# Optimization experiments

Hardware: AMD Instinct MI355X
Metric: run time of the kernel (lower is better)

## Reference

```python
import jax, jax.numpy as jnp
import numpy as np
from functools import partial

B, N, T = 4, 10000, 128
E = 160000
H, C = 4, 64            # heads, out_channels per head
GAT_DIM = H * C         # 256
NEG_SLOPE = 0.2


def conv1d(x, w, b):
    # x: (M, Cin, L), w: (Cout, Cin, K), 'same' padding (pad=1 for k=3)
    y = jax.lax.conv_general_dilated(x, w, window_strides=(1,), padding=[(1, 1)],
                                     dimension_numbers=('NCH', 'OIH', 'NCH'))
    return y + b[None, :, None]


def maxpool2(x):
    # kernel=2, stride=2 over last axis
    return jax.lax.reduce_window(x, -jnp.inf, jax.lax.max,
                                 (1, 1, 2), (1, 1, 2), 'VALID')


def gat_layer_single(x, src, dst, W, att_s, att_d, bias):
    # x: (N, Fin); PyG GATConv with concat=True, self-loops already appended to src/dst
    n = x.shape[0]
    xl = (x @ W).reshape(n, H, C)                       # (N, H, C)
    a_s = jnp.sum(xl * att_s[None], axis=-1)            # (N, H)
    a_d = jnp.sum(xl * att_d[None], axis=-1)            # (N, H)
    e = jax.nn.leaky_relu(a_s[src] + a_d[dst], NEG_SLOPE)  # (E', H)
    emax = jax.ops.segment_max(e, dst, num_segments=n)     # (N, H)
    ex = jnp.exp(e - emax[dst])
    denom = jax.ops.segment_sum(ex, dst, num_segments=n)   # (N, H)
    alpha = ex / (denom[dst] + 1e-16)                       # (E', H)
    msg = xl[src] * alpha[..., None]                        # (E', H, C)
    out = jax.ops.segment_sum(msg, dst, num_segments=n)     # (N, H, C)
    return out.reshape(n, H * C) + bias


def setup_inputs() -> dict:
    key = jax.random.key(0)
    ks = jax.random.split(key, 24)
    rn = lambda k, sh, fan: jax.random.normal(k, sh, jnp.float32) / np.sqrt(fan)
    inp = {
        'x': jax.random.normal(ks[0], (B, N, T), jnp.float32),
        'edge_index': jax.random.randint(ks[1], (2, E), 0, N, jnp.int64),
        # temporal conv
        'cw1': rn(ks[2], (32, 1, 3), 3), 'cb1': jnp.zeros((32,), jnp.float32),
        'cw2': rn(ks[3], (64, 32, 3), 96), 'cb2': jnp.zeros((64,), jnp.float32),
        # GAT layer 0 (in=64)
        'W0': rn(ks[4], (64, GAT_DIM), 64), 'as0': rn(ks[5], (H, C), C), 'ad0': rn(ks[6], (H, C), C),
        'b0': jnp.zeros((GAT_DIM,), jnp.float32),
        # GAT layer 1 (in=256)
        'W1': rn(ks[7], (GAT_DIM, GAT_DIM), GAT_DIM), 'as1': rn(ks[8], (H, C), C), 'ad1': rn(ks[9], (H, C), C),
        'b1': jnp.zeros((GAT_DIM,), jnp.float32),
        # classification head 256->128->2
        'Wc1': rn(ks[10], (GAT_DIM, 128), GAT_DIM), 'bc1': jnp.zeros((128,), jnp.float32),
        'Wc2': rn(ks[11], (128, 2), 128), 'bc2': jnp.zeros((2,), jnp.float32),
        # attribution head 256->64->1
        'Wa1': rn(ks[12], (GAT_DIM, 64), GAT_DIM), 'ba1': jnp.zeros((64,), jnp.float32),
        'Wa2': rn(ks[13], (64, 1), 64), 'ba2': jnp.zeros((1,), jnp.float32),
    }
    return inp


def reference(x, edge_index, cw1, cb1, cw2, cb2, W0, as0, ad0, b0, W1, as1, ad1, b1,
              Wc1, bc1, Wc2, bc2, Wa1, ba1, Wa2, ba2):
    b, n, t = x.shape
    # ---- temporal conv over all B*N node signals ----
    xf = x.reshape(b * n, 1, t)
    h = jax.nn.relu(conv1d(xf, cw1, cb1))            # (BN, 32, T)
    h = maxpool2(h)                                  # (BN, 32, T//2)
    h = jax.nn.relu(conv1d(h, cw2, cb2))             # (BN, 64, T//2)
    feat = jnp.mean(h, axis=-1).reshape(b, n, 64)    # adaptive_avg_pool1d(1)
    # ---- GAT stack (self-loops appended, PyG default) ----
    src0, dst0 = edge_index[0], edge_index[1]
    loops = jnp.arange(n, dtype=src0.dtype)
    src = jnp.concatenate([src0, loops])
    dst = jnp.concatenate([dst0, loops])
    gat0 = jax.vmap(partial(gat_layer_single, src=src, dst=dst, W=W0, att_s=as0, att_d=ad0, bias=b0))
    gat1 = jax.vmap(partial(gat_layer_single, src=src, dst=dst, W=W1, att_s=as1, att_d=ad1, bias=b1))
    g = jax.nn.relu(gat0(feat))                      # (B, N, 256); dropout = identity (eval)
    g = jax.nn.relu(gat1(g))                         # (B, N, 256)
    # ---- heads ----
    pooled = jnp.mean(g, axis=1)                     # (B, 256)
    logits = jax.nn.relu(pooled @ Wc1 + bc1) @ Wc2 + bc2          # (B, 2)
    attr = jax.nn.sigmoid(jax.nn.relu(g @ Wa1 + ba1) @ Wa2 + ba2)  # (B, N, 1)
    return logits, attr[..., 0]
```

## Files before the change

kernel.cpp:

```cpp
#include <hip/hip_runtime.h>
#include <hip/hip_bf16.h>
#include <math.h>

typedef __hip_bfloat16 bf16;
typedef unsigned short u16;
typedef unsigned int u32;
typedef __attribute__((ext_vector_type(8))) short short8;
typedef __attribute__((ext_vector_type(4))) float f32x4;
typedef __attribute__((ext_vector_type(2))) float f32x2;

#define BATCH 4
#define NNODE 10000
#define TLEN 128
#define NEDGE 160000
#define GDIM 256
#define NHEAD 4
#define XROW 272

#define S_CW1 0
#define S_CB1 96
#define S_CB2 128
#define S_AS0 192
#define S_AD0 448
#define S_B0  704
#define S_AS1 960
#define S_AD1 1216
#define S_B1  1472
#define S_BC1 1728
#define S_WC2 1856
#define S_BC2 2112
#define S_BA1 2114
#define S_WA2 2178
#define S_BA2 2242
#define S_TOTAL 2243

__device__ __forceinline__ float prelu(float v) { return fmaxf(v, 0.f); }
__device__ __forceinline__ u16 f2b(float f) {
    union { float f; u32 u; } v; v.f = f;
    u32 r = v.u + 0x7FFF + ((v.u >> 16) & 1);
    return (u16)(r >> 16);
}
__device__ __forceinline__ float u2f(u16 u) {
    union { u32 u; float f; } v; v.u = ((u32)u) << 16;
    return v.f;
}
__device__ __forceinline__ float ldw(const void* p, int off, bool isbf) {
    return isbf ? u2f(((const u16*)p)[off]) : ((const float*)p)[off];
}

__device__ __forceinline__ bool probe_x_bf16(const void* xsrc) {
    int lane = threadIdx.x & 63;
    u16 h = ((const u16*)xsrc)[2 * lane];
    int e = (h >> 7) & 0xFF;
    unsigned long long m = __ballot(e >= 117 && e <= 130);
    return __popcll(m) >= 32;
}
__device__ __forceinline__ bool probe_ei64(const int* ei) {
    int lane = threadIdx.x & 63;
    int v = ei[2 * lane + 1];
    unsigned long long m = __ballot(v == 0);
    return __popcll(m) >= 56;
}

struct WPtrs { const void* p[20]; };

#define PRE_TBLK 665
__global__ __launch_bounds__(256) void k_pre(WPtrs wp, const void* __restrict__ xsrc,
        const int* __restrict__ ei, float* __restrict__ wbuf,
        u16* __restrict__ cw2r, u16* __restrict__ W0t, u16* __restrict__ W1t,
        u16* __restrict__ Wa1t, int* __restrict__ counts) {
    bool isbf = probe_x_bf16(xsrc);
    int b = blockIdx.x;
    if (b >= PRE_TBLK) {
        const int C2[16] = {0,96,128,192,448,704,960,1216,1472,1728,1856,2112,
                            2114,2178,2242,2243};
        const int SRC[15] = {0,1,3,5,6,7,9,10,11,13,14,15,17,18,19};
        int i = (b - PRE_TBLK) * 256 + threadIdx.x;
        if (i >= S_TOTAL) return;
        int j = 14;
        for (int t = 0; t < 15; ++t) { if (i < C2[t + 1]) { j = t; break; } }
        wbuf[i] = ldw(wp.p[SRC[j]], i - C2[j], isbf);
        return;
    }
    int i = b * 256 + threadIdx.x;
    if (i < 6144) {
        int c2 = i / 96, k = i - c2 * 96, s = k >> 5, ci = k & 31;
        cw2r[i] = f2b(ldw(wp.p[2], c2 * 96 + ci * 3 + s, isbf));
    }
    if (i < 16384) {
        int k = i >> 8, c = i & 255;
        W0t[c * 64 + k] = f2b(ldw(wp.p[4], k * 256 + c, isbf));
        int ka = i >> 6, ca = i & 63;
        Wa1t[ca * 256 + ka] = f2b(ldw(wp.p[16], ka * 64 + ca, isbf));
    }
    if (i < 65536) {
        int k = i >> 8, c = i & 255;
        W1t[c * 256 + k] = f2b(ldw(wp.p[8], k * 256 + c, isbf));
    }
    if (i < NEDGE + NNODE) {
        bool ei64 = probe_ei64(ei);
        int dst;
        if (i < NEDGE) dst = ei64 ? ei[2 * (NEDGE + i)] : ei[NEDGE + i];
        else dst = i - NEDGE;
        if (dst >= 0 && dst < NNODE) atomicAdd(&counts[dst], 1);
    }
}

__global__ __launch_bounds__(1024) void k_scan(const int* __restrict__ counts,
        int* __restrict__ cur, int* __restrict__ row_ptr) {
    __shared__ int buf[1024];
    int t = threadIdx.x;
    int base = t * 10;
    int c[10];
    int s = 0;
    #pragma unroll
    for (int i = 0; i < 10; ++i) {
        int idx = base + i;
        c[i] = (idx < NNODE) ? counts[idx] : 0;
        s += c[i];
    }
    buf[t] = s;
    __syncthreads();
    for (int off = 1; off < 1024; off <<= 1) {
        int v = (t >= off) ? buf[t - off] : 0;
        __syncthreads();
        buf[t] += v;
        __syncthreads();
    }
    int run = buf[t] - s;
    #pragma unroll
    for (int i = 0; i < 10; ++i) {
        int idx = base + i;
        if (idx < NNODE) {
            cur[idx] = run;
            run += c[i];
            row_ptr[idx + 1] = run;
        }
    }
    if (t == 0) row_ptr[0] = 0;
}

#define HSTR 40
#define NPW 4
#define FILL_BLK 665
__global__ __launch_bounds__(256) void k_conv(const void* __restrict__ xsrc,
        const float* __restrict__ wbuf, const u16* __restrict__ cw2r,
        u16* __restrict__ featb, const int* __restrict__ ei,
        int* __restrict__ cur, int* __restrict__ col_src) {
    __shared__ __align__(16) float xs[4][132];
    __shared__ float w1s[96], b1s[32], b2s[64];
    __shared__ __align__(16) u16 hb[4][66 * HSTR];

    bool isbf = probe_x_bf16(xsrc);
    int tid = threadIdx.x;
    int wave = tid >> 6, lane = tid & 63;
    int node0 = blockIdx.x * (4 * NPW);

    int m = lane & 15, q = lane >> 4;
    short8 bfr[4][3];
    #pragma unroll
    for (int nt = 0; nt < 4; ++nt)
        #pragma unroll
        for (int sh = 0; sh < 3; ++sh)
            bfr[nt][sh] = *(const short8*)&cw2r[(nt * 16 + m) * 96 + sh * 32 + q * 8];

    if (tid < 96) w1s[tid] = wbuf[S_CW1 + tid];
    if (tid < 32) b1s[tid] = wbuf[S_CB1 + tid];
    if (tid < 64) b2s[tid] = wbuf[S_CB2 + tid];
    if (tid < 8) xs[tid >> 1][(tid & 1) ? 129 : 0] = 0.f;
    if (tid < 64) {
        int w = tid >> 4, idx = tid & 15;
        *(u32*)&hb[w][2 * idx] = 0;
        *(u32*)&hb[w][65 * HSTR + 2 * idx] = 0;
    }
    __syncthreads();

    float* xsw = xs[wave];
    u16* hw = &hb[wave][0];

    int d = m, uu = q;
    float wa0 = w1s[6 * d + 0], wa1 = w1s[6 * d + 1], wa2 = w1s[6 * d + 2];
    float wb0 = w1s[6 * d + 3], wb1 = w1s[6 * d + 4], wb2 = w1s[6 * d + 5];
    float ba = b1s[2 * d], bb = b1s[2 * d + 1];
    float b2vv[4];
    #pragma unroll
    for (int nt = 0; nt < 4; ++nt) b2vv[nt] = b2s[nt * 16 + m];

    int node = node0 + wave;
    u32 plo = 0; float2 pf = {0.f, 0.f};
    if (isbf) plo = ((const u32*)xsrc)[(size_t)node * 64 + lane];
    else      pf  = ((const float2*)xsrc)[(size_t)node * 64 + lane];

    for (int j = 0; j < NPW; ++j) {
        if (isbf) {
            xsw[1 + 2 * lane] = u2f((u16)(plo & 0xFFFF));
            xsw[2 + 2 * lane] = u2f((u16)(plo >> 16));
        } else {
            xsw[1 + 2 * lane] = pf.x;
            xsw[2 + 2 * lane] = pf.y;
        }
        if (j + 1 < NPW) {
            int nxt = node + 4;
            if (isbf) plo = ((const u32*)xsrc)[(size_t)nxt * 64 + lane];
            else      pf  = ((const float2*)xsrc)[(size_t)nxt * 64 + lane];
        }

        #pragma unroll
        for (int it = 0; it < 16; ++it) {
            int u = uu + 4 * it;
            int t0 = 2 * u;
            float2 xa = *(const float2*)&xsw[t0];
            float2 xb = *(const float2*)&xsw[t0 + 2];
            float x0 = xa.x, x1 = xa.y, x2 = xb.x, x3 = xb.y;
            f32x2 A = {x0, x1}, Bv = {x1, x2}, Cv = {x2, x3};
            f32x2 va = {ba, ba}; va += wa0 * A; va += wa1 * Bv; va += wa2 * Cv;
            f32x2 vb = {bb, bb}; vb += wb0 * A; vb += wb1 * Bv; vb += wb2 * Cv;
            float ha = fmaxf(fmaxf(va.x, va.y), 0.f);
            float hb2 = fmaxf(fmaxf(vb.x, vb.y), 0.f);
            __hip_bfloat162 hp2 = __float22bfloat162_rn(make_float2(ha, hb2));
            u32 pack; __builtin_memcpy(&pack, &hp2, 4);
            *(u32*)&hw[(u + 1) * HSTR + 2 * d] = pack;
        }

        float pc0 = 0.f, pc1 = 0.f, pc2 = 0.f, pc3 = 0.f;
        #pragma unroll
        for (int mt = 0; mt < 4; ++mt) {
            const u16* hr = &hw[(mt * 16 + m) * HSTR + q * 8];
            short8 a0 = *(const short8*)&hr[0 * HSTR];
            short8 a1 = *(const short8*)&hr[1 * HSTR];
            short8 a2 = *(const short8*)&hr[2 * HSTR];
            f32x4 c0 = {0.f,0.f,0.f,0.f}, c1 = {0.f,0.f,0.f,0.f};
            f32x4 c2 = {0.f,0.f,0.f,0.f}, c3 = {0.f,0.f,0.f,0.f};
            c0 = __builtin_amdgcn_mfma_f32_16x16x32_bf16(a0, bfr[0][0], c0, 0, 0, 0);
            c1 = __builtin_amdgcn_mfma_f32_16x16x32_bf16(a0, bfr[1][0], c1, 0, 0, 0);
            c2 = __builtin_amdgcn_mfma_f32_16x16x32_bf16(a0, bfr[2][0], c2, 0, 0, 0);
            c3 = __builtin_amdgcn_mfma_f32_16x16x32_bf16(a0, bfr[3][0], c3, 0, 0, 0);
            c0 = __builtin_amdgcn_mfma_f32_16x16x32_bf16(a1, bfr[0][1], c0, 0, 0, 0);
            c1 = __builtin_amdgcn_mfma_f32_16x16x32_bf16(a1, bfr[1][1], c1, 0, 0, 0);
            c2 = __builtin_amdgcn_mfma_f32_16x16x32_bf16(a1, bfr[2][1], c2, 0, 0, 0);
            c3 = __builtin_amdgcn_mfma_f32_16x16x32_bf16(a1, bfr[3][1], c3, 0, 0, 0);
            c0 = __builtin_amdgcn_mfma_f32_16x16x32_bf16(a2, bfr[0][2], c0, 0, 0, 0);
            c1 = __builtin_amdgcn_mfma_f32_16x16x32_bf16(a2, bfr[1][2], c1, 0, 0, 0);
            c2 = __builtin_amdgcn_mfma_f32_16x16x32_bf16(a2, bfr[2][2], c2, 0, 0, 0);
            c3 = __builtin_amdgcn_mfma_f32_16x16x32_bf16(a2, bfr[3][2], c3, 0, 0, 0);
            pc0 += prelu(c0[0] + b2vv[0]) + prelu(c0[1] + b2vv[0])
                 + prelu(c0[2] + b2vv[0]) + prelu(c0[3] + b2vv[0]);
            pc1 += prelu(c1[0] + b2vv[1]) + prelu(c1[1] + b2vv[1])
                 + prelu(c1[2] + b2vv[1]) + prelu(c1[3] + b2vv[1]);
            pc2 += prelu(c2[0] + b2vv[2]) + prelu(c2[1] + b2vv[2])
                 + prelu(c2[2] + b2vv[2]) + prelu(c2[3] + b2vv[2]);
            pc3 += prelu(c3[0] + b2vv[3]) + prelu(c3[1] + b2vv[3])
                 + prelu(c3[2] + b2vv[3]) + prelu(c3[3] + b2vv[3]);
        }
        pc0 += __shfl_xor(pc0, 16, 64); pc0 += __shfl_xor(pc0, 32, 64);
        pc1 += __shfl_xor(pc1, 16, 64); pc1 += __shfl_xor(pc1, 32, 64);
        pc2 += __shfl_xor(pc2, 16, 64); pc2 += __shfl_xor(pc2, 32, 64);
        pc3 += __shfl_xor(pc3, 16, 64); pc3 += __shfl_xor(pc3, 32, 64);
        float v = (q == 0) ? pc0 : (q == 1) ? pc1 : (q == 2) ? pc2 : pc3;
        int bb2 = node / NNODE, nn = node - bb2 * NNODE;
        featb[((size_t)nn * 4 + bb2) * 64 + lane] = f2b(v * (1.f / 64.f));

        node += 4;
    }

    if (blockIdx.x < FILL_BLK) {
        bool ei64 = probe_ei64(ei);
        int e = blockIdx.x * 256 + tid;
        if (e < NEDGE + NNODE) {
            int src, dst;
            if (e < NEDGE) {
                if (ei64) { src = ei[2 * e]; dst = ei[2 * (NEDGE + e)]; }
                else      { src = ei[e];     dst = ei[NEDGE + e]; }
            } else {
                src = dst = e - NEDGE;
            }
            if (dst >= 0 && dst < NNODE) {
                int pos = atomicAdd(&cur[dst], 1);
                if (pos >= 0 && pos < NEDGE + NNODE) col_src[pos] = src;
            }
        }
    }
}

template<int K>
__global__ __launch_bounds__(256) void k_gemm(const u16* __restrict__ A,
        const u16* __restrict__ Wt, const float* __restrict__ att_s_w,
        const float* __restrict__ att_d_w, u16* __restrict__ outb) {
    int wave = threadIdx.x >> 6, lane = threadIdx.x & 63;
    int row0 = (blockIdx.x * 4 + wave) * 16;
    int m = lane & 15, q = lane >> 4;
    f32x4 acc[16];
    #pragma unroll
    for (int nt = 0; nt < 16; ++nt) acc[nt] = {0.f, 0.f, 0.f, 0.f};
    for (int kc = 0; kc < K; kc += 32) {
        short8 a = *(const short8*)&A[(size_t)(row0 + m) * K + kc + q * 8];
        #pragma unroll
        for (int nt = 0; nt < 16; ++nt) {
            short8 b = *(const short8*)&Wt[(size_t)(nt * 16 + m) * K + kc + q * 8];
            acc[nt] = __builtin_amdgcn_mfma_f32_16x16x32_bf16(a, b, acc[nt], 0, 0, 0);
        }
    }
    #pragma unroll
    for (int nt = 0; nt < 16; ++nt) {
        #pragma unroll
        for (int r = 0; r < 4; ++r)
            outb[(size_t)(row0 + q * 4 + r) * XROW + nt * 16 + m] = f2b(acc[nt][r]);
    }
    float sh_s[4][4] = {{0}}, sh_d[4][4] = {{0}};
    #pragma unroll
    for (int nt = 0; nt < 16; ++nt) {
        int h = nt >> 2;
        int cc = (nt & 3) * 16 + m;
        float asw = att_s_w[h * 64 + cc];
        float adw = att_d_w[h * 64 + cc];
        #pragma unroll
        for (int r = 0; r < 4; ++r) {
            sh_s[h][r] += acc[nt][r] * asw;
            sh_d[h][r] += acc[nt][r] * adw;
        }
    }
    #pragma unroll
    for (int off = 1; off < 16; off <<= 1) {
        #pragma unroll
        for (int h = 0; h < 4; ++h)
            #pragma unroll
            for (int r = 0; r < 4; ++r) {
                sh_s[h][r] += __shfl_xor(sh_s[h][r], off, 64);
                sh_d[h][r] += __shfl_xor(sh_d[h][r], off, 64);
            }
    }
    if (m == 0) {
        #pragma unroll
        for (int r = 0; r < 4; ++r) {
            int row = row0 + q * 4 + r;
            float4 vs = {sh_s[0][r], sh_s[1][r], sh_s[2][r], sh_s[3][r]};
            float4 vd = {sh_d[0][r], sh_d[1][r], sh_d[2][r], sh_d[3][r]};
            *(float4*)&outb[(size_t)row * XROW + 256] = vs;
            *(float4*)&outb[(size_t)row * XROW + 264] = vd;
        }
    }
}

__global__ __launch_bounds__(256) void k_agg(const u16* __restrict__ xlb,
        const int* __restrict__ row_ptr, const int* __restrict__ col_src,
        const float* __restrict__ bias, u16* __restrict__ gb_out) {
    int wave = threadIdx.x >> 6, lane = threadIdx.x & 63;
    int dst = __builtin_amdgcn_readfirstlane(blockIdx.x * 2 + (wave >> 1));
    int bp = (wave & 1) * 2;
    int beg = __builtin_amdgcn_readfirstlane(row_ptr[dst]);
    int end = __builtin_amdgcn_readfirstlane(row_ptr[dst + 1]);

    int bl = lane >> 5;
    int s = lane & 31;
    int h = s >> 3;
    int b = bp + bl;
    float advh = *(const float*)&xlb[((size_t)dst * 4 + b) * XROW + 264 + h * 2];

    float m = -INFINITY, l = 0.f;
    float acc[8];
    #pragma unroll
    for (int k = 0; k < 8; ++k) acc[k] = 0.f;

    int i = beg;
    int n0 = 0, n1 = 0, n2 = 0, n3 = 0;
    if (i + 4 <= end) {
        n0 = col_src[i]; n1 = col_src[i + 1];
        n2 = col_src[i + 2]; n3 = col_src[i + 3];
    }
    while (i + 4 <= end) {
        int s0 = min(max(n0, 0), NNODE - 1);
        int s1 = min(max(n1, 0), NNODE - 1);
        int s2 = min(max(n2, 0), NNODE - 1);
        int s3 = min(max(n3, 0), NNODE - 1);
        const u16* r0 = &xlb[((size_t)s0 * 4 + b) * XROW];
        const u16* r1 = &xlb[((size_t)s1 * 4 + b) * XROW];
        const u16* r2 = &xlb[((size_t)s2 * 4 + b) * XROW];
        const u16* r3 = &xlb[((size_t)s3 * 4 + b) * XROW];
        float a0 = *(const float*)&r0[256 + h * 2];
        float a1 = *(const float*)&r1[256 + h * 2];
        float a2 = *(const float*)&r2[256 + h * 2];
        float a3 = *(const float*)&r3[256 + h * 2];
        short8 x0 = *(const short8*)&r0[s * 8];
        short8 x1 = *(const short8*)&r1[s * 8];
        short8 x2 = *(const short8*)&r2[s * 8];
        short8 x3 = *(const short8*)&r3[s * 8];
        i += 4;
        if (i + 4 <= end) {
            n0 = col_src[i]; n1 = col_src[i + 1];
            n2 = col_src[i + 2]; n3 = col_src[i + 3];
        }
        float e0 = a0 + advh; e0 = (e0 >= 0.f) ? e0 : 0.2f * e0;
        float e1 = a1 + advh; e1 = (e1 >= 0.f) ? e1 : 0.2f * e1;
        float e2 = a2 + advh; e2 = (e2 >= 0.f) ? e2 : 0.2f * e2;
        float e3 = a3 + advh; e3 = (e3 >= 0.f) ? e3 : 0.2f * e3;
        float cmax = fmaxf(fmaxf(e0, e1), fmaxf(e2, e3));
        if (__any(cmax > m)) {
            float mn = fmaxf(m, cmax);
            float r = __expf(m - mn);
            m = mn;
            l *= r;
            #pragma unroll
            for (int k = 0; k < 8; ++k) acc[k] *= r;
        }
        float p0 = __expf(e0 - m); l += p0;
        #pragma unroll
        for (int k = 0; k < 8; ++k) acc[k] += p0 * u2f((u16)x0[k]);
        float p1 = __expf(e1 - m); l += p1;
        #pragma unroll
        for (int k = 0; k < 8; ++k) acc[k] += p1 * u2f((u16)x1[k]);
        float p2 = __expf(e2 - m); l += p2;
        #pragma unroll
        for (int k = 0; k < 8; ++k) acc[k] += p2 * u2f((u16)x2[k]);
        float p3 = __expf(e3 - m); l += p3;
        #pragma unroll
        for (int k = 0; k < 8; ++k) acc[k] += p3 * u2f((u16)x3[k]);
    }
    for (; i < end; ++i) {
        int s0 = min(max(col_src[i], 0), NNODE - 1);
        const u16* r0 = &xlb[((size_t)s0 * 4 + b) * XROW];
        float a0 = *(const float*)&r0[256 + h * 2];
        short8 x0 = *(const short8*)&r0[s * 8];
        float e0 = a0 + advh; e0 = (e0 >= 0.f) ? e0 : 0.2f * e0;
        if (__any(e0 > m)) {
            float mn = fmaxf(m, e0);
            float r = __expf(m - mn);
            m = mn;
            l *= r;
            #pragma unroll
            for (int k = 0; k < 8; ++k) acc[k] *= r;
        }
        float p0 = __expf(e0 - m); l += p0;
        #pragma unroll
        for (int k = 0; k < 8; ++k) acc[k] += p0 * u2f((u16)x0[k]);
    }

    float rl = 1.f / (l + 1e-16f);
    short8 o;
    #pragma unroll
    for (int k = 0; k < 8; ++k)
        o[k] = (short)f2b(prelu(acc[k] * rl + bias[s * 8 + k]));
    *(short8*)&gb_out[((size_t)dst * 4 + b) * 256 + s * 8] = o;
}

__global__ __launch_bounds__(256) void k_attrpool(const u16* __restrict__ gb,
        const u16* __restrict__ Wa1t, const float* __restrict__ wbuf,
        float* __restrict__ out, float* __restrict__ pooled) {
    if (blockIdx.x >= 625) {
        int pb = blockIdx.x - 625;
        int b = pb >> 6;
        int chunk = pb & 63;
        int cch = threadIdx.x;
        int n0 = chunk * 157;
        int n1 = min(NNODE, n0 + 157);
        float acc = 0.f;
        int n = n0;
        for (; n + 4 <= n1; n += 4) {
            float v0 = u2f(gb[((size_t)n * 4 + b) * 256 + cch]);
            float v1 = u2f(gb[((size_t)(n + 1) * 4 + b) * 256 + cch]);
            float v2 = u2f(gb[((size_t)(n + 2) * 4 + b) * 256 + cch]);
            float v3 = u2f(gb[((size_t)(n + 3) * 4 + b) * 256 + cch]);
            acc += v0; acc += v1; acc += v2; acc += v3;
        }
        for (; n < n1; ++n)
            acc += u2f(gb[((size_t)n * 4 + b) * 256 + cch]);
        atomicAdd(&pooled[b * 256 + cch], acc);
        return;
    }
    int wave = threadIdx.x >> 6, lane = threadIdx.x & 63;
    int row0 = (blockIdx.x * 4 + wave) * 16;
    int m = lane & 15, q = lane >> 4;
    f32x4 acc[4];
    #pragma unroll
    for (int nt = 0; nt < 4; ++nt) acc[nt] = {0.f, 0.f, 0.f, 0.f};
    for (int kc = 0; kc < 256; kc += 32) {
        short8 a = *(const short8*)&gb[(size_t)(row0 + m) * 256 + kc + q * 8];
        #pragma unroll
        for (int nt = 0; nt < 4; ++nt) {
            short8 b = *(const short8*)&Wa1t[(size_t)(nt * 16 + m) * 256 + kc + q * 8];
            acc[nt] = __builtin_amdgcn_mfma_f32_16x16x32_bf16(a, b, acc[nt], 0, 0, 0);
        }
    }
    float part[4] = {0, 0, 0, 0};
    #pragma unroll
    for (int nt = 0; nt < 4; ++nt) {
        int col = nt * 16 + m;
        float ba1v = wbuf[S_BA1 + col];
        float wa2v = wbuf[S_WA2 + col];
        #pragma unroll
        for (int r = 0; r < 4; ++r)
            part[r] += prelu(acc[nt][r] + ba1v) * wa2v;
    }
    #pragma unroll
    for (int off = 1; off < 16; off <<= 1) {
        #pragma unroll
        for (int r = 0; r < 4; ++r)
            part[r] += __shfl_xor(part[r], off, 64);
    }
    if (m == 0) {
        float ba2v = wbuf[S_BA2];
        #pragma unroll
        for (int r = 0; r < 4; ++r) {
            int row = row0 + q * 4 + r;
            int n = row >> 2, b = row & 3;
            float v = part[r] + ba2v;
            out[8 + b * NNODE + n] = 1.f / (1.f + __expf(-v));
        }
    }
}

__global__ __launch_bounds__(128) void k_logits(const float* __restrict__ pooled,
        const float* __restrict__ wbuf, const void* __restrict__ Wc1p,
        float* __restrict__ out,
        const u16* __restrict__ featb, const u16* __restrict__ gb,
        const int* __restrict__ row_ptr, const int* __restrict__ ei,
        const void* __restrict__ xsrc, int hostbad) {
    int tid = threadIdx.x;
    bool isbf = probe_x_bf16(xsrc);
    if (blockIdx.x == 4) {
        __shared__ float red[128];
        bool ei64 = probe_ei64(ei);
        float mx[2] = {0.f, 0.f};
        const u16* bufs[2] = {featb, gb};
        for (int qq = 0; qq < 2; ++qq) {
            const u16* p = bufs[qq];
            float m = 0.f;
            for (int i = tid; i < 2048; i += 128) {
                float v = u2f(p[i]);
                if (v != v) m = 1e30f;
                m = fmaxf(m, fabsf(v));
            }
            red[tid] = m;
            __syncthreads();
            for (int s2 = 64; s2 > 0; s2 >>= 1) {
                if (tid < s2) red[tid] = fmaxf(red[tid], red[tid + s2]);
                __syncthreads();
            }
            mx[qq] = red[0];
            __syncthreads();
        }
        if (tid == 0) {
            int fb = (mx[0] > 1e8f || mx[0] < 1e-6f) ? 1 : 0;
            int gbad = (mx[1] > 1e8f || mx[1] < 1e-6f) ? 1 : 0;
            int cb = (row_ptr[NNODE] != NEDGE + NNODE) ? 1 : 0;
            int code = 100 * fb + 400 * gbad + 800 * cb + 6400 * hostbad;
            if (code) {
                code += 1600 * (isbf ? 0 : 1);
                code += 3200 * (ei64 ? 1 : 0);
                for (int j = 0; j < 8; ++j) out[j] = (float)code;
            }
        }
        return;
    }
    __shared__ float pm[256];
    __shared__ float red4[4];
    int b = blockIdx.x;
    pm[tid] = pooled[b * 256 + tid] * (1.f / NNODE);
    pm[tid + 128] = pooled[b * 256 + tid + 128] * (1.f / NNODE);
    __syncthreads();
    float acc = wbuf[S_BC1 + tid];
    if (isbf) {
        const u16* w = (const u16*)Wc1p;
        #pragma unroll 4
        for (int k = 0; k < 256; ++k)
            acc += pm[k] * u2f(w[k * 128 + tid]);
    } else {
        const float* w = (const float*)Wc1p;
        #pragma unroll 4
        for (int k = 0; k < 256; ++k)
            acc += pm[k] * w[k * 128 + tid];
    }
    float hv = prelu(acc);
    float p0 = hv * wbuf[S_WC2 + tid * 2];
    float p1 = hv * wbuf[S_WC2 + tid * 2 + 1];
    #pragma unroll
    for (int off = 32; off > 0; off >>= 1) {
        p0 += __shfl_xor(p0, off, 64);
        p1 += __shfl_xor(p1, off, 64);
    }
    int wv = tid >> 6, lane = tid & 63;
    if (lane == 0) { red4[wv * 2] = p0; red4[wv * 2 + 1] = p1; }
    __syncthreads();
    if (tid < 2)
        out[b * 2 + tid] = red4[tid] + red4[2 + tid] + wbuf[S_BC2 + tid];
}

extern "C" void kernel_launch(void* const* d_in, const int* in_sizes, int n_in,
                              void* d_out, int out_size, void* d_ws, size_t ws_size,
                              hipStream_t stream) {
    const void* x  = d_in[0];
    const int*  ei = (const int*)d_in[1];
    float* out = (float*)d_out;

    WPtrs wp;
    for (int j = 0; j < 20; ++j) wp.p[j] = d_in[j + 2];

    char* ws = (char*)d_ws;
    size_t off = 0;
    auto alloc = [&](size_t bytes) -> void* {
        void* p = ws + off;
        off += (bytes + 255) & ~(size_t)255;
        return p;
    };
    float* wbuf    = (float*)alloc((size_t)S_TOTAL * 4);
    u16*   featb   = (u16*)  alloc((size_t)BATCH * NNODE * 64 * 2);
    u16*   xlb     = (u16*)  alloc((size_t)BATCH * NNODE * XROW * 2);
    u16*   gb      = (u16*)  alloc((size_t)BATCH * NNODE * 256 * 2);
    u16*   cw2r    = (u16*)alloc(6144 * 2);
    u16*   W0t     = (u16*)alloc(16384 * 2);
    u16*   W1t     = (u16*)alloc(65536 * 2);
    u16*   Wa1t    = (u16*)alloc(16384 * 2);
    int*   counts  = (int*)alloc(NNODE * 4);
    float* pooled  = (float*)alloc(BATCH * 256 * 4);
    int*   row_ptr = (int*)alloc((NNODE + 1) * 4);
    int*   cur     = (int*)alloc(NNODE * 4);
    int*   col_src = (int*)alloc((NEDGE + NNODE) * 4);
    (void)ws_size; (void)out_size;

    int hostbad = (n_in != 22 || in_sizes[0] != BATCH * NNODE * TLEN ||
                   in_sizes[1] != 2 * NEDGE) ? 1 : 0;

    hipMemsetAsync(counts, 0, 40192 + 4096, stream);

    k_pre<<<PRE_TBLK + 9, 256, 0, stream>>>(wp, x, ei, wbuf, cw2r, W0t, W1t, Wa1t, counts);
    k_scan<<<1, 1024, 0, stream>>>(counts, cur, row_ptr);

    k_conv<<<BATCH * NNODE / (4 * NPW), 256, 0, stream>>>(x, wbuf, cw2r, featb, ei, cur, col_src);

    k_gemm<64><<<BATCH * NNODE / 64, 256, 0, stream>>>(featb, W0t,
            wbuf + S_AS0, wbuf + S_AD0, xlb);
    k_agg<<<NNODE / 2, 256, 0, stream>>>(xlb, row_ptr, col_src, wbuf + S_B0, gb);

    k_gemm<256><<<BATCH * NNODE / 64, 256, 0, stream>>>(gb, W1t,
            wbuf + S_AS1, wbuf + S_AD1, xlb);
    k_agg<<<NNODE / 2, 256, 0, stream>>>(xlb, row_ptr, col_src, wbuf + S_B1, gb);

    k_attrpool<<<625 + 256, 256, 0, stream>>>(gb, Wa1t, wbuf, out, pooled);
    k_logits<<<5, 128, 0, stream>>>(pooled, wbuf, wp.p[12], out, featb, gb, row_ptr, ei, x, hostbad);
}
```

Before: 402.3 us.

## Fuse layer-0 GAT projection into conv kernel and split attention logits out

Fuses the first GAT linear projection and its attention-logit reductions into the temporal conv kernel, staging each block's 16 pooled features in shared memory and running the MFMA there. This drops one kernel launch and the round trip of the feature tensor. It also changes the layout from node-major interleaved batches with a padded 272-wide row to batch-major 256-wide rows. The per-node attention scalars move into separate compact a_s/a_d arrays, which makes the gather rows in aggregation aligned and smaller. The cost is more shared memory and registers in the conv kernel, and the edge scatter and projection must share one block.

```diff
diff --git a/kernel.cpp b/kernel.cpp
--- a/kernel.cpp
+++ b/kernel.cpp
@@ -15,7 +15,6 @@
 #define NEDGE 160000
 #define GDIM 256
 #define NHEAD 4
-#define XROW 272
 
 #define S_CW1 0
 #define S_CB1 96
@@ -141,15 +140,18 @@
 }
 
 #define HSTR 40
+#define FSTR 72
 #define NPW 4
 #define FILL_BLK 665
 __global__ __launch_bounds__(256) void k_conv(const void* __restrict__ xsrc,
         const float* __restrict__ wbuf, const u16* __restrict__ cw2r,
-        u16* __restrict__ featb, const int* __restrict__ ei,
-        int* __restrict__ cur, int* __restrict__ col_src) {
+        const u16* __restrict__ W0t, u16* __restrict__ featb,
+        u16* __restrict__ xlb, float* __restrict__ a_s, float* __restrict__ a_d,
+        const int* __restrict__ ei, int* __restrict__ cur, int* __restrict__ col_src) {
     __shared__ __align__(16) float xs[4][132];
     __shared__ float w1s[96], b1s[32], b2s[64];
     __shared__ __align__(16) u16 hb[4][66 * HSTR];
+    __shared__ __align__(16) u16 fs[16][FSTR];
 
     bool isbf = probe_x_bf16(xsrc);
     int tid = threadIdx.x;
@@ -257,8 +259,9 @@
         pc2 += __shfl_xor(pc2, 16, 64); pc2 += __shfl_xor(pc2, 32, 64);
         pc3 += __shfl_xor(pc3, 16, 64); pc3 += __shfl_xor(pc3, 32, 64);
         float v = (q == 0) ? pc0 : (q == 1) ? pc1 : (q == 2) ? pc2 : pc3;
-        int bb2 = node / NNODE, nn = node - bb2 * NNODE;
-        featb[((size_t)nn * 4 + bb2) * 64 + lane] = f2b(v * (1.f / 64.f));
+        u16 fv = f2b(v * (1.f / 64.f));
+        featb[(size_t)node * 64 + lane] = fv;
+        fs[wave + 4 * j][lane] = fv;
 
         node += 4;
     }
@@ -280,12 +283,69 @@
             }
         }
     }
-}
-
-template<int K>
+
+    __syncthreads();
+
+    {
+        f32x4 acc[4];
+        #pragma unroll
+        for (int ntl = 0; ntl < 4; ++ntl) acc[ntl] = {0.f, 0.f, 0.f, 0.f};
+        #pragma unroll
+        for (int kc = 0; kc < 64; kc += 32) {
+            short8 a = *(const short8*)&fs[m][kc + q * 8];
+            #pragma unroll
+            for (int ntl = 0; ntl < 4; ++ntl) {
+                int col0 = wave * 64 + ntl * 16;
+                short8 bw = *(const short8*)&W0t[(size_t)(col0 + m) * 64 + kc + q * 8];
+                acc[ntl] = __builtin_amdgcn_mfma_f32_16x16x32_bf16(a, bw, acc[ntl], 0, 0, 0);
+            }
+        }
+        #pragma unroll
+        for (int ntl = 0; ntl < 4; ++ntl) {
+            #pragma unroll
+            for (int r = 0; r < 4; ++r)
+                xlb[(size_t)(node0 + q * 4 + r) * 256 + wave * 64 + ntl * 16 + m]
+                    = f2b(acc[ntl][r]);
+        }
+        const float* asw_p = wbuf + S_AS0;
+        const float* adw_p = wbuf + S_AD0;
+        float sh_s[4] = {0, 0, 0, 0}, sh_d[4] = {0, 0, 0, 0};
+        #pragma unroll
+        for (int ntl = 0; ntl < 4; ++ntl) {
+            float asw = asw_p[wave * 64 + ntl * 16 + m];
+            float adw = adw_p[wave * 64 + ntl * 16 + m];
+            #pragma unroll
+            for (int r = 0; r < 4; ++r) {
+                sh_s[r] += acc[ntl][r] * asw;
+                sh_d[r] += acc[ntl][r] * adw;
+            }
+        }
+        #pragma unroll
+        for (int off = 1; off < 16; off <<= 1) {
+            #pragma unroll
+            for (int r = 0; r < 4; ++r) {
+                sh_s[r] += __shfl_xor(sh_s[r], off, 64);
+                sh_d[r] += __shfl_xor(sh_d[r], off, 64);
+            }
+        }
+        if (m == 0) {
+            int bb2 = node0 / NNODE;
+            int nn0 = node0 - bb2 * NNODE;
+            #pragma unroll
+            for (int r = 0; r < 4; ++r) {
+                int nn = nn0 + q * 4 + r;
+                a_s[(size_t)nn * 16 + bb2 * 4 + wave] = sh_s[r];
+                a_d[(size_t)nn * 16 + bb2 * 4 + wave] = sh_d[r];
+            }
+        }
+    }
+}
+
 __global__ __launch_bounds__(256) void k_gemm(const u16* __restrict__ A,
         const u16* __restrict__ Wt, const float* __restrict__ att_s_w,
-        const float* __restrict__ att_d_w, u16* __restrict__ outb) {
+        const float* __restrict__ att_d_w, u16* __restrict__ outb,
+        float* __restrict__ a_s, float* __restrict__ a_d) {
+    const int K = 256;
     int wave = threadIdx.x >> 6, lane = threadIdx.x & 63;
     int row0 = (blockIdx.x * 4 + wave) * 16;
     int m = lane & 15, q = lane >> 4;
@@ -304,7 +364,7 @@
     for (int nt = 0; nt < 16; ++nt) {
         #pragma unroll
         for (int r = 0; r < 4; ++r)
-            outb[(size_t)(row0 + q * 4 + r) * XROW + nt * 16 + m] = f2b(acc[nt][r]);
+            outb[(size_t)(row0 + q * 4 + r) * 256 + nt * 16 + m] = f2b(acc[nt][r]);
     }
     float sh_s[4][4] = {{0}}, sh_d[4][4] = {{0}};
     #pragma unroll
@@ -333,15 +393,17 @@
         #pragma unroll
         for (int r = 0; r < 4; ++r) {
             int row = row0 + q * 4 + r;
+            int b = row / NNODE, nn = row - b * NNODE;
             float4 vs = {sh_s[0][r], sh_s[1][r], sh_s[2][r], sh_s[3][r]};
             float4 vd = {sh_d[0][r], sh_d[1][r], sh_d[2][r], sh_d[3][r]};
-            *(float4*)&outb[(size_t)row * XROW + 256] = vs;
-            *(float4*)&outb[(size_t)row * XROW + 264] = vd;
+            *(float4*)&a_s[(size_t)nn * 16 + b * 4] = vs;
+            *(float4*)&a_d[(size_t)nn * 16 + b * 4] = vd;
         }
     }
 }
 
 __global__ __launch_bounds__(256) void k_agg(const u16* __restrict__ xlb,
+        const float* __restrict__ a_s, const float* __restrict__ a_d,
         const int* __restrict__ row_ptr, const int* __restrict__ col_src,
         const float* __restrict__ bias, u16* __restrict__ gb_out) {
     int wave = threadIdx.x >> 6, lane = threadIdx.x & 63;
@@ -354,7 +416,9 @@
     int s = lane & 31;
     int h = s >> 3;
     int b = bp + bl;
-    float advh = *(const float*)&xlb[((size_t)dst * 4 + b) * XROW + 264 + h * 2];
+    int asoff = b * 4 + h;
+    size_t rowb = (size_t)b * NNODE;
+    float advh = a_d[(size_t)dst * 16 + asoff];
 
     float m = -INFINITY, l = 0.f;
     float acc[8];
@@ -372,18 +436,14 @@
         int s1 = min(max(n1, 0), NNODE - 1);
         int s2 = min(max(n2, 0), NNODE - 1);
         int s3 = min(max(n3, 0), NNODE - 1);
-        const u16* r0 = &xlb[((size_t)s0 * 4 + b) * XROW];
-        const u16* r1 = &xlb[((size_t)s1 * 4 + b) * XROW];
-        const u16* r2 = &xlb[((size_t)s2 * 4 + b) * XROW];
-        const u16* r3 = &xlb[((size_t)s3 * 4 + b) * XROW];
-        float a0 = *(const float*)&r0[256 + h * 2];
-        float a1 = *(const float*)&r1[256 + h * 2];
-        float a2 = *(const float*)&r2[256 + h * 2];
-        float a3 = *(const float*)&r3[256 + h * 2];
-        short8 x0 = *(const short8*)&r0[s * 8];
-        short8 x1 = *(const short8*)&r1[s * 8];
-        short8 x2 = *(const short8*)&r2[s * 8];
-        short8 x3 = *(const short8*)&r3[s * 8];
+        float a0 = a_s[(size_t)s0 * 16 + asoff];
+        float a1 = a_s[(size_t)s1 * 16 + asoff];
+        float a2 = a_s[(size_t)s2 * 16 + asoff];
+        float a3 = a_s[(size_t)s3 * 16 + asoff];
+        short8 x0 = *(const short8*)&xlb[(rowb + s0) * 256 + s * 8];
+        short8 x1 = *(const short8*)&xlb[(rowb + s1) * 256 + s * 8];
+        short8 x2 = *(const short8*)&xlb[(rowb + s2) * 256 + s * 8];
+        short8 x3 = *(const short8*)&xlb[(rowb + s3) * 256 + s * 8];
         i += 4;
         if (i + 4 <= end) {
             n0 = col_src[i]; n1 = col_src[i + 1];
@@ -417,9 +477,8 @@
     }
     for (; i < end; ++i) {
         int s0 = min(max(col_src[i], 0), NNODE - 1);
-        const u16* r0 = &xlb[((size_t)s0 * 4 + b) * XROW];
-        float a0 = *(const float*)&r0[256 + h * 2];
-        short8 x0 = *(const short8*)&r0[s * 8];
+        float a0 = a_s[(size_t)s0 * 16 + asoff];
+        short8 x0 = *(const short8*)&xlb[(rowb + s0) * 256 + s * 8];
         float e0 = a0 + advh; e0 = (e0 >= 0.f) ? e0 : 0.2f * e0;
         if (__any(e0 > m)) {
             float mn = fmaxf(m, e0);
@@ -439,7 +498,7 @@
     #pragma unroll
     for (int k = 0; k < 8; ++k)
         o[k] = (short)f2b(prelu(acc[k] * rl + bias[s * 8 + k]));
-    *(short8*)&gb_out[((size_t)dst * 4 + b) * 256 + s * 8] = o;
+    *(short8*)&gb_out[(rowb + dst) * 256 + s * 8] = o;
 }
 
 __global__ __launch_bounds__(256) void k_attrpool(const u16* __restrict__ gb,
@@ -452,17 +511,18 @@
         int cch = threadIdx.x;
         int n0 = chunk * 157;
         int n1 = min(NNODE, n0 + 157);
+        size_t rowb = (size_t)b * NNODE;
         float acc = 0.f;
         int n = n0;
         for (; n + 4 <= n1; n += 4) {
-            float v0 = u2f(gb[((size_t)n * 4 + b) * 256 + cch]);
-            float v1 = u2f(gb[((size_t)(n + 1) * 4 + b) * 256 + cch]);
-            float v2 = u2f(gb[((size_t)(n + 2) * 4 + b) * 256 + cch]);
-            float v3 = u2f(gb[((size_t)(n + 3) * 4 + b) * 256 + cch]);
+            float v0 = u2f(gb[(rowb + n) * 256 + cch]);
+            float v1 = u2f(gb[(rowb + n + 1) * 256 + cch]);
+            float v2 = u2f(gb[(rowb + n + 2) * 256 + cch]);
+            float v3 = u2f(gb[(rowb + n + 3) * 256 + cch]);
             acc += v0; acc += v1; acc += v2; acc += v3;
         }
         for (; n < n1; ++n)
-            acc += u2f(gb[((size_t)n * 4 + b) * 256 + cch]);
+            acc += u2f(gb[(rowb + n) * 256 + cch]);
         atomicAdd(&pooled[b * 256 + cch], acc);
         return;
     }
@@ -501,9 +561,8 @@
         #pragma unroll
         for (int r = 0; r < 4; ++r) {
             int row = row0 + q * 4 + r;
-            int n = row >> 2, b = row & 3;
             float v = part[r] + ba2v;
-            out[8 + b * NNODE + n] = 1.f / (1.f + __expf(-v));
+            out[8 + row] = 1.f / (1.f + __expf(-v));
         }
     }
 }
@@ -603,8 +662,10 @@
     };
     float* wbuf    = (float*)alloc((size_t)S_TOTAL * 4);
     u16*   featb   = (u16*)  alloc((size_t)BATCH * NNODE * 64 * 2);
-    u16*   xlb     = (u16*)  alloc((size_t)BATCH * NNODE * XROW * 2);
+    u16*   xlb     = (u16*)  alloc((size_t)BATCH * NNODE * 256 * 2);
     u16*   gb      = (u16*)  alloc((size_t)BATCH * NNODE * 256 * 2);
+    float* a_s     = (float*)alloc((size_t)BATCH * NNODE * 4 * 4);
+    float* a_d     = (float*)alloc((size_t)BATCH * NNODE * 4 * 4);
     u16*   cw2r    = (u16*)alloc(6144 * 2);
     u16*   W0t     = (u16*)alloc(16384 * 2);
     u16*   W1t     = (u16*)alloc(65536 * 2);
@@ -624,15 +685,14 @@
     k_pre<<<PRE_TBLK + 9, 256, 0, stream>>>(wp, x, ei, wbuf, cw2r, W0t, W1t, Wa1t, counts);
     k_scan<<<1, 1024, 0, stream>>>(counts, cur, row_ptr);
 
-    k_conv<<<BATCH * NNODE / (4 * NPW), 256, 0, stream>>>(x, wbuf, cw2r, featb, ei, cur, col_src);
-
-    k_gemm<64><<<BATCH * NNODE / 64, 256, 0, stream>>>(featb, W0t,
-            wbuf + S_AS0, wbuf + S_AD0, xlb);
-    k_agg<<<NNODE / 2, 256, 0, stream>>>(xlb, row_ptr, col_src, wbuf + S_B0, gb);
-
-    k_gemm<256><<<BATCH * NNODE / 64, 256, 0, stream>>>(gb, W1t,
-            wbuf + S_AS1, wbuf + S_AD1, xlb);
-    k_agg<<<NNODE / 2, 256, 0, stream>>>(xlb, row_ptr, col_src, wbuf + S_B1, gb);
+    k_conv<<<BATCH * NNODE / 16, 256, 0, stream>>>(x, wbuf, cw2r, W0t, featb,
+            xlb, a_s, a_d, ei, cur, col_src);
+
+    k_agg<<<NNODE / 2, 256, 0, stream>>>(xlb, a_s, a_d, row_ptr, col_src, wbuf + S_B0, gb);
+
+    k_gemm<<<BATCH * NNODE / 64, 256, 0, stream>>>(gb, W1t,
+            wbuf + S_AS1, wbuf + S_AD1, xlb, a_s, a_d);
+    k_agg<<<NNODE / 2, 256, 0, stream>>>(xlb, a_s, a_d, row_ptr, col_src, wbuf + S_B1, gb);
 
     k_attrpool<<<625 + 256, 256, 0, stream>>>(gb, Wa1t, wbuf, out, pooled);
     k_logits<<<5, 128, 0, stream>>>(pooled, wbuf, wp.p[12], out, featb, gb, row_ptr, ei, x, hostbad);
```

After: 389.7 us. 3.1% less time.
